# Kernel optimization log

Measured on AMD Instinct MI355X. Metric: run time of the kernel, lower is better.

The kernel has to match this reference:

```python
import jax, jax.numpy as jnp
import numpy as np
import math

B, T, H, W, D = 64, 512, 128, 128, 32


def _lin(k, out, inn):
    k1, k2 = jax.random.split(k)
    lim = 1.0 / np.sqrt(inn)
    return (jax.random.uniform(k1, (out, inn), jnp.float32, -lim, lim),
            jax.random.uniform(k2, (out,), jnp.float32, -lim, lim))


def setup_inputs() -> dict:
    key = jax.random.key(0)
    ks = jax.random.split(key, 12)
    ts = jnp.broadcast_to(jnp.linspace(0.0, 4.0 * math.pi, T, dtype=jnp.float32), (B, T))
    coef = lambda k: jax.random.normal(k, (B, T - 1, D), jnp.float32) * 0.1
    i_W0, i_b0 = _lin(ks[4], W, D)
    i_W1, i_b1 = _lin(ks[5], W, W)
    i_W2, i_b2 = _lin(ks[6], H, W)
    f_W0, f_b0 = _lin(ks[7], W, H)
    f_W1, f_b1 = _lin(ks[8], W, W)
    f_W2, f_b2 = _lin(ks[9], H * D, W)
    l_W, l_b = _lin(ks[10], 1, H)
    return dict(ts=ts,
                coeff_d=coef(ks[0]), coeff_c=coef(ks[1]), coeff_b=coef(ks[2]), coeff_a=coef(ks[3]),
                i_W0=i_W0, i_b0=i_b0, i_W1=i_W1, i_b1=i_b1, i_W2=i_W2, i_b2=i_b2,
                f_W0=f_W0, f_b0=f_b0, f_W1=f_W1, f_b1=f_b1, f_W2=f_W2, f_b2=f_b2,
                l_W=l_W, l_b=l_b)


def reference(ts, coeff_d, coeff_c, coeff_b, coeff_a,
              i_W0, i_b0, i_W1, i_b1, i_W2, i_b2,
              f_W0, f_b0, f_W1, f_b1, f_W2, f_b2,
              l_W, l_b):
    def initial_mlp(x):  # eqx.nn.MLP default: relu hidden, identity final
        x = jax.nn.relu(i_W0 @ x + i_b0)
        x = jax.nn.relu(i_W1 @ x + i_b1)
        return i_W2 @ x + i_b2

    def func_mlp(y):  # softplus hidden, tanh final, reshape (H, D)
        h = jax.nn.softplus(f_W0 @ y + f_b0)
        h = jax.nn.softplus(f_W1 @ h + f_b1)
        return jnp.tanh(f_W2 @ h + f_b2).reshape(H, D)

    def single(ts_i, d, c, b, a):
        dt = ts_i[1] - ts_i[0]
        y0 = initial_mlp(a[0])  # control.evaluate(ts[0]) = a[0] (frac=0 in first interval)

        def deriv(t):  # diffrax CubicInterpolation.derivative
            idx = jnp.clip(jnp.searchsorted(ts_i, t, side='right') - 1, 0, ts_i.shape[0] - 2)
            frac = t - ts_i[idx]
            return b[idx] + frac * (2.0 * c[idx] + frac * 3.0 * d[idx])

        def f(t, y):  # ControlTerm.to_ode() vf_prod with control=dt
            return (func_mlp(y) @ deriv(t)) * dt

        def step(carry, _):  # ralston_step_fn
            t0, y = carry
            k1 = f(t0, y)
            k2 = f(t0 + 0.5 * dt, y + 0.5 * k1)
            k3 = f(t0 + 0.75 * dt, y + 0.75 * k2)
            y1 = (2.0 / 9.0 * k1 + 1.0 / 3.0 * k2 + 4.0 / 9.0 * k3) * dt + y
            return (t0 + dt, y1), y1

        _, ys = jax.lax.scan(step, (ts_i[0], y0), None, length=ts_i.shape[0])
        return jax.nn.sigmoid(ys @ l_W[0] + l_b[0])  # (T,), evolving_out=True

    return jax.vmap(single)(ts, coeff_d, coeff_c, coeff_b, coeff_a)
```

## Files before the change

### kernel.cpp

```cpp
#include <hip/hip_runtime.h>
#include <hip/hip_bf16.h>

#define TT 512
#define BB 64
#define HH 128
#define WW 128
#define DD 32
#define NTHR 512
#define CSTRIDE 16352

#define SMEM_BYTES 86016

typedef __attribute__((ext_vector_type(8))) short short8;
typedef __attribute__((ext_vector_type(4))) float f32x4;

__device__ __forceinline__ float softplus_f(float x) {
    return fmaxf(x, 0.f) + __logf(1.f + __expf(-fabsf(x)));
}
__device__ __forceinline__ float fast_tanh(float x) {
    float ax = fabsf(x);
    float e  = __expf(-2.f * ax);
    float r  = (1.f - e) * __builtin_amdgcn_rcpf(1.f + e);
    return copysignf(r, x);
}
__device__ __forceinline__ short bf16rne(float x) {
    unsigned u = __float_as_uint(x);
    u += 0x7fffu + ((u >> 16) & 1u);
    return (short)(u >> 16);
}
__device__ __forceinline__ void store_l2(unsigned long long* p, unsigned long long v) {
    asm volatile("global_store_dwordx2 %0, %1, off sc0"
                 :: "v"(p), "v"(v) : "memory");
}
__device__ __forceinline__ unsigned long long load_l2(const unsigned long long* p) {
    unsigned long long v;
    asm volatile("global_load_dwordx2 %0, %1, off sc0\n\t"
                 "s_waitcnt vmcnt(0)"
                 : "=v"(v) : "v"(p) : "memory");
    return v;
}

__global__ __launch_bounds__(NTHR, 2)
void cde_kernel(const float* __restrict__ ts,
                const float* __restrict__ cd, const float* __restrict__ cc,
                const float* __restrict__ cb, const float* __restrict__ ca,
                const float* __restrict__ iW0, const float* __restrict__ ib0,
                const float* __restrict__ iW1, const float* __restrict__ ib1,
                const float* __restrict__ iW2, const float* __restrict__ ib2,
                const float* __restrict__ fW0, const float* __restrict__ fb0,
                const float* __restrict__ fW1, const float* __restrict__ fb1,
                const float* __restrict__ fW2, const float* __restrict__ fb2,
                const float* __restrict__ lW, const float* __restrict__ lb,
                unsigned* __restrict__ xcdctr,
                float* camb,
                unsigned long long* kslow,
                float* __restrict__ out)
{
    extern __shared__ float sm[];
    float* tss    = sm;
    float* ybuf   = tss + TT;
    float* dvec   = ybuf + 128;
    float* scr    = dvec + 96;
    float* klocal = scr + 256;
    short* ybf    = (short*)(klocal + 32);
    short* h1bf   = ybf + 128;
    short* h2bf   = h1bf + 128;
    int*   clm    = (int*)(h2bf + 128);

    const int tid  = threadIdx.x;
    const int lane = tid & 63;
    const int wv   = tid >> 6;
    const int quad = lane >> 4;
    const int qr   = lane & 15;

    if (tid == 0) {
        unsigned xcc;
        asm volatile("s_getreg_b32 %0, hwreg(HW_REG_XCC_ID)" : "=s"(xcc));
        xcc &= 7u;
        unsigned slot = atomicAdd(&xcdctr[xcc], 1u);
        clm[0] = (int)(xcc * 8u + (slot >> 2));
        clm[1] = (int)(slot & 3u);
    }
    __syncthreads();
    const int b = clm[0];
    const int m = clm[1];

    unsigned long long* kfast =
        (unsigned long long*)(camb + (size_t)b * CSTRIDE + 2048);

    const int cg = qr & 3;
    const int ct = (qr >> 2) & 1;
    const int rh = qr >> 3;
    const int dbase = ct * 16 + quad * 4 + rh * 2;

    for (int i = tid; i < TT; i += NTHR) tss[i] = ts[(size_t)b * TT + i];

    short8 afr[4][8];
    #pragma unroll
    for (int gi = 0; gi < 4; ++gi) {
        int g = m * 32 + wv * 4 + gi;
        #pragma unroll
        for (int t = 0; t < 2; ++t)
        #pragma unroll
        for (int K = 0; K < 4; ++K) {
            int row = g * 32 + t * 16 + qr;
            int col = K * 32 + quad * 8;
            const float* src = fW2 + (size_t)row * WW + col;
            short8 v;
            #pragma unroll
            for (int j = 0; j < 8; ++j) v[j] = bf16rne(src[j]);
            afr[gi][t * 4 + K] = v;
        }
    }
    short8 w0f[4], w1f[4];
    #pragma unroll
    for (int K = 0; K < 4; ++K) {
        int row = wv * 16 + qr;
        int col = K * 32 + quad * 8;
        const float* s0 = fW0 + (size_t)row * HH + col;
        const float* s1 = fW1 + (size_t)row * WW + col;
        short8 v0, v1;
        #pragma unroll
        for (int j = 0; j < 8; ++j) { v0[j] = bf16rne(s0[j]); v1[j] = bf16rne(s1[j]); }
        w0f[K] = v0; w1f[K] = v1;
    }
    const float fb0r = fb0[wv * 16 + quad * 4 + cg];
    const float fb1r = fb1[wv * 16 + quad * 4 + cg];
    const int   hrow = m * 32 + wv * 4 + cg;
    const float fb2a = fb2[hrow * 32 + dbase];
    const float fb2b = fb2[hrow * 32 + dbase + 1];

    __syncthreads();

    const float dt = tss[1] - tss[0];
    float t00 = tss[0];
    const size_t cstride = (size_t)CSTRIDE;
    const float* cdb = cd + (size_t)b * cstride;
    const float* ccb = cc + (size_t)b * cstride;
    const float* cbb = cb + (size_t)b * cstride;

    if (tid < HH) {
        const float* a0 = ca + (size_t)b * cstride;
        float acc = ib0[tid];
        #pragma unroll
        for (int k = 0; k < DD; ++k) acc += iW0[tid * DD + k] * a0[k];
        scr[tid] = fmaxf(acc, 0.f);
    }
    __syncthreads();
    if (tid < HH) {
        float acc = ib1[tid];
        for (int k = 0; k < WW; ++k) acc += iW1[tid * WW + k] * scr[k];
        scr[128 + tid] = fmaxf(acc, 0.f);
    }
    __syncthreads();
    float yreg = 0.f, k1r = 0.f, k2r = 0.f;
    if (tid < HH) {
        float acc = ib2[tid];
        for (int k = 0; k < WW; ++k) acc += iW2[tid * WW + k] * scr[128 + k];
        yreg = acc;
        ybuf[tid] = acc;
        ybf[tid]  = bf16rne(acc);
    }
    __syncthreads();

    float lwa = 0.f, lwb = 0.f, lbv = 0.f;
    if (wv == 0) { lwa = lW[lane]; lwb = lW[64 + lane]; lbv = lb[0]; }

    for (int s = 0; s < TT; ++s) {
        if (wv < 3) {
            float tv = t00 + ((wv == 0) ? 0.f : (wv == 1) ? 0.5f : 0.75f) * dt;
            int cnt = 0;
            #pragma unroll
            for (int ch = 0; ch < 8; ++ch)
                cnt += __popcll(__ballot(tss[ch * 64 + lane] <= tv));
            int idx = min(max(cnt - 1, 0), TT - 2);
            if (lane < DD) {
                float frac = tv - tss[idx];
                size_t o = (size_t)idx * DD + lane;
                dvec[wv * 32 + lane] =
                    cbb[o] + frac * (2.f * ccb[o] + frac * 3.f * cdb[o]);
            }
        }

        #pragma unroll 1
        for (int q = 0; q < 3; ++q) {
            const int gen = s * 3 + q + 1;
            const int buf = gen & 1;

            {
                f32x4 aA = {0.f, 0.f, 0.f, 0.f}, aB = {0.f, 0.f, 0.f, 0.f};
                short8 b0 = *(const short8*)(ybf + 0 * 32 + quad * 8);
                short8 b1 = *(const short8*)(ybf + 1 * 32 + quad * 8);
                short8 b2 = *(const short8*)(ybf + 2 * 32 + quad * 8);
                short8 b3 = *(const short8*)(ybf + 3 * 32 + quad * 8);
                aA = __builtin_amdgcn_mfma_f32_16x16x32_bf16(w0f[0], b0, aA, 0, 0, 0);
                aB = __builtin_amdgcn_mfma_f32_16x16x32_bf16(w0f[1], b1, aB, 0, 0, 0);
                aA = __builtin_amdgcn_mfma_f32_16x16x32_bf16(w0f[2], b2, aA, 0, 0, 0);
                aB = __builtin_amdgcn_mfma_f32_16x16x32_bf16(w0f[3], b3, aB, 0, 0, 0);
                f32x4 h = aA + aB;
                if (qr < 4) {
                    float v = (qr & 1) ? ((qr & 2) ? h[3] : h[1])
                                       : ((qr & 2) ? h[2] : h[0]);
                    h1bf[wv * 16 + quad * 4 + qr] = bf16rne(softplus_f(v + fb0r));
                }
            }
            __syncthreads();
            {
                f32x4 aA = {0.f, 0.f, 0.f, 0.f}, aB = {0.f, 0.f, 0.f, 0.f};
                short8 b0 = *(const short8*)(h1bf + 0 * 32 + quad * 8);
                short8 b1 = *(const short8*)(h1bf + 1 * 32 + quad * 8);
                short8 b2 = *(const short8*)(h1bf + 2 * 32 + quad * 8);
                short8 b3 = *(const short8*)(h1bf + 3 * 32 + quad * 8);
                aA = __builtin_amdgcn_mfma_f32_16x16x32_bf16(w1f[0], b0, aA, 0, 0, 0);
                aB = __builtin_amdgcn_mfma_f32_16x16x32_bf16(w1f[1], b1, aB, 0, 0, 0);
                aA = __builtin_amdgcn_mfma_f32_16x16x32_bf16(w1f[2], b2, aA, 0, 0, 0);
                aB = __builtin_amdgcn_mfma_f32_16x16x32_bf16(w1f[3], b3, aB, 0, 0, 0);
                f32x4 h = aA + aB;
                if (qr < 4) {
                    float v = (qr & 1) ? ((qr & 2) ? h[3] : h[1])
                                       : ((qr & 2) ? h[2] : h[0]);
                    h2bf[wv * 16 + quad * 4 + qr] = bf16rne(softplus_f(v + fb1r));
                }
            }
            __syncthreads();

            {
                short8 bfr[4];
                #pragma unroll
                for (int K = 0; K < 4; ++K)
                    bfr[K] = *(const short8*)(h2bf + K * 32 + quad * 8);
                f32x4 A0[4], A1[4];
                #pragma unroll
                for (int gi = 0; gi < 4; ++gi) {
                    f32x4 a0 = {0.f, 0.f, 0.f, 0.f};
                    f32x4 a1 = {0.f, 0.f, 0.f, 0.f};
                    a0 = __builtin_amdgcn_mfma_f32_16x16x32_bf16(afr[gi][0], bfr[0], a0, 0, 0, 0);
                    a0 = __builtin_amdgcn_mfma_f32_16x16x32_bf16(afr[gi][1], bfr[1], a0, 0, 0, 0);
                    a0 = __builtin_amdgcn_mfma_f32_16x16x32_bf16(afr[gi][2], bfr[2], a0, 0, 0, 0);
                    a0 = __builtin_amdgcn_mfma_f32_16x16x32_bf16(afr[gi][3], bfr[3], a0, 0, 0, 0);
                    a1 = __builtin_amdgcn_mfma_f32_16x16x32_bf16(afr[gi][4], bfr[0], a1, 0, 0, 0);
                    a1 = __builtin_amdgcn_mfma_f32_16x16x32_bf16(afr[gi][5], bfr[1], a1, 0, 0, 0);
                    a1 = __builtin_amdgcn_mfma_f32_16x16x32_bf16(afr[gi][6], bfr[2], a1, 0, 0, 0);
                    a1 = __builtin_amdgcn_mfma_f32_16x16x32_bf16(afr[gi][7], bfr[3], a1, 0, 0, 0);
                    A0[gi] = a0; A1[gi] = a1;
                }
                f32x4 s0a = (cg & 1) ? A0[1] : A0[0];
                f32x4 s0b = (cg & 1) ? A0[3] : A0[2];
                f32x4 s0  = (cg & 2) ? s0b : s0a;
                f32x4 s1a = (cg & 1) ? A1[1] : A1[0];
                f32x4 s1b = (cg & 1) ? A1[3] : A1[2];
                f32x4 s1  = (cg & 2) ? s1b : s1a;
                f32x4 st  = ct ? s1 : s0;
                float va = rh ? st[2] : st[0];
                float vb = rh ? st[3] : st[1];
                float2 dv = *(const float2*)(dvec + q * 32 + dbase);
                float p = fast_tanh(va + fb2a) * dv.x + fast_tanh(vb + fb2b) * dv.y;
                p += __shfl_xor(p, 8);
                p += __shfl_xor(p, 4);
                p += __shfl_xor(p, 16);
                p += __shfl_xor(p, 32);
                if (lane < 4) {
                    const float kval = p * dt;
                    const size_t off = (size_t)buf * HH + m * 32 + wv * 4 + lane;
                    unsigned long long pk =
                        ((unsigned long long)__float_as_uint(kval) << 32) | (unsigned)gen;
                    klocal[wv * 4 + lane] = kval;
                    store_l2(kfast + off, pk);
                    __hip_atomic_store(&kslow[(size_t)(buf * BB + b) * HH + m * 32 + wv * 4 + lane],
                                       pk, __ATOMIC_RELAXED, __HIP_MEMORY_SCOPE_AGENT);
                }
            }
            __syncthreads();

            if (tid < HH) {
                float kv;
                const int rel = tid - m * 32;
                if (rel >= 0 && rel < 32) {
                    kv = klocal[rel];
                } else {
                    unsigned long long v;
                    int it = 0;
                    for (;;) {
                        if ((it & 1) == 0) {
                            v = load_l2(kfast + (size_t)buf * HH + tid);
                        } else {
                            v = __hip_atomic_load(&kslow[(size_t)(buf * BB + b) * HH + tid],
                                                  __ATOMIC_RELAXED, __HIP_MEMORY_SCOPE_AGENT);
                        }
                        if ((unsigned)v == (unsigned)gen) break;
                        if (++it > 128) __builtin_amdgcn_s_sleep(1);
                    }
                    kv = __uint_as_float((unsigned)(v >> 32));
                }
                float nxt;
                if (q == 0)      { k1r = kv; nxt = yreg + 0.5f  * kv; }
                else if (q == 1) { k2r = kv; nxt = yreg + 0.75f * kv; }
                else {
                    nxt = yreg + dt * ((2.f/9.f) * k1r + (1.f/3.f) * k2r + (4.f/9.f) * kv);
                    yreg = nxt;
                    ybuf[tid] = nxt;
                }
                ybf[tid] = bf16rne(nxt);
            }
            __syncthreads();
        }

        if (m == 0 && wv == 0) {
            float p = ybuf[lane] * lwa + ybuf[64 + lane] * lwb;
            p += __shfl_xor(p, 1);  p += __shfl_xor(p, 2);  p += __shfl_xor(p, 4);
            p += __shfl_xor(p, 8);  p += __shfl_xor(p, 16); p += __shfl_xor(p, 32);
            if (lane == 0) out[(size_t)b * TT + s] = 1.f / (1.f + __expf(-(p + lbv)));
        }
        t00 += dt;
    }
}

extern "C" void kernel_launch(void* const* d_in, const int* in_sizes, int n_in,
                              void* d_out, int out_size, void* d_ws, size_t ws_size,
                              hipStream_t stream) {
    const float* ts  = (const float*)d_in[0];
    const float* cdp = (const float*)d_in[1];
    const float* ccp = (const float*)d_in[2];
    const float* cbp = (const float*)d_in[3];
    const float* cap = (const float*)d_in[4];
    const float* iW0 = (const float*)d_in[5];
    const float* ib0 = (const float*)d_in[6];
    const float* iW1 = (const float*)d_in[7];
    const float* ib1 = (const float*)d_in[8];
    const float* iW2 = (const float*)d_in[9];
    const float* ib2 = (const float*)d_in[10];
    const float* fW0 = (const float*)d_in[11];
    const float* fb0 = (const float*)d_in[12];
    const float* fW1 = (const float*)d_in[13];
    const float* fb1 = (const float*)d_in[14];
    const float* fW2 = (const float*)d_in[15];
    const float* fb2 = (const float*)d_in[16];
    const float* lW  = (const float*)d_in[17];
    const float* lb  = (const float*)d_in[18];
    float* out = (float*)d_out;

    unsigned* xcdctr = (unsigned*)d_ws;
    unsigned long long* kslow = (unsigned long long*)((char*)d_ws + 256);
    hipMemsetAsync(d_ws, 0, 256 + (size_t)2 * BB * HH * sizeof(unsigned long long), stream);

    hipFuncSetAttribute((const void*)cde_kernel,
                        hipFuncAttributeMaxDynamicSharedMemorySize, SMEM_BYTES);
    hipLaunchKernelGGL(cde_kernel, dim3(256), dim3(NTHR), SMEM_BYTES, stream,
                       ts, cdp, ccp, cbp, cap, iW0, ib0, iW1, ib1, iW2, ib2,
                       fW0, fb0, fW1, fb1, fW2, fb2, lW, lb, xcdctr,
                       (float*)cap, kslow, out);
}
```

Measured before the change: 3.558 ms.

## Replicate y state per wave and poll k values directly, removing two block barriers

Each wave now keeps its own copy of the 128-element y vector in registers and in a private LDS slab. Every wave polls all k values from the global exchange buffer, including its own block's values, and updates its copy itself. This removes the two __syncthreads per RK stage that surrounded the single-warp gather and update. The cost is eight times more global polling traffic per block and redundant y updates in every wave. Correctness still depends on wave-local LDS ordering and on the gen-tagged buffer double-buffering being safe without a block barrier.

New measurement: 10.40 ms. 192% more time.

```diff
diff --git a/kernel.cpp b/kernel.cpp
--- a/kernel.cpp
+++ b/kernel.cpp
@@ -32,12 +32,34 @@
     asm volatile("global_store_dwordx2 %0, %1, off sc0"
                  :: "v"(p), "v"(v) : "memory");
 }
-__device__ __forceinline__ unsigned long long load_l2(const unsigned long long* p) {
-    unsigned long long v;
-    asm volatile("global_load_dwordx2 %0, %1, off sc0\n\t"
-                 "s_waitcnt vmcnt(0)"
-                 : "=v"(v) : "v"(p) : "memory");
-    return v;
+
+__device__ __forceinline__ void poll_pair(const unsigned long long* f0,
+                                          const unsigned long long* s0,
+                                          unsigned gen, float& kv0, float& kv1) {
+    unsigned long long v0 = 0, v1 = 0;
+    bool d0 = false, d1 = false;
+    int it = 0;
+    for (;;) {
+        unsigned long long a, b;
+        asm volatile("global_load_dwordx2 %0, %2, off sc0\n\t"
+                     "global_load_dwordx2 %1, %3, off sc0\n\t"
+                     "s_waitcnt vmcnt(0)"
+                     : "=&v"(a), "=&v"(b)
+                     : "v"(f0), "v"(f0 + 64) : "memory");
+        if ((unsigned)a == gen) { v0 = a; d0 = true; }
+        if ((unsigned)b == gen) { v1 = b; d1 = true; }
+        if (d0 && d1) break;
+        if (++it > 24) {
+            a = __hip_atomic_load(s0,      __ATOMIC_RELAXED, __HIP_MEMORY_SCOPE_AGENT);
+            b = __hip_atomic_load(s0 + 64, __ATOMIC_RELAXED, __HIP_MEMORY_SCOPE_AGENT);
+            if ((unsigned)a == gen) { v0 = a; d0 = true; }
+            if ((unsigned)b == gen) { v1 = b; d1 = true; }
+            if (d0 && d1) break;
+            __builtin_amdgcn_s_sleep(1);
+        }
+    }
+    kv0 = __uint_as_float((unsigned)(v0 >> 32));
+    kv1 = __uint_as_float((unsigned)(v1 >> 32));
 }
 
 __global__ __launch_bounds__(NTHR, 2)
@@ -58,20 +80,20 @@
 {
     extern __shared__ float sm[];
     float* tss    = sm;
-    float* ybuf   = tss + TT;
-    float* dvec   = ybuf + 128;
+    float* dvec   = tss + TT;
     float* scr    = dvec + 96;
-    float* klocal = scr + 256;
-    short* ybf    = (short*)(klocal + 32);
-    short* h1bf   = ybf + 128;
+    float* yini   = scr + 256;
+    short* h1bf   = (short*)(yini + 128);
     short* h2bf   = h1bf + 128;
-    int*   clm    = (int*)(h2bf + 128);
+    short* ybp    = h2bf + 128;
+    int*   clm    = (int*)(ybp + 8 * 128);
 
     const int tid  = threadIdx.x;
     const int lane = tid & 63;
     const int wv   = tid >> 6;
     const int quad = lane >> 4;
     const int qr   = lane & 15;
+    short* myslab  = ybp + wv * 128;
 
     if (tid == 0) {
         unsigned xcc;
@@ -153,15 +175,18 @@
         scr[128 + tid] = fmaxf(acc, 0.f);
     }
     __syncthreads();
-    float yreg = 0.f, k1r = 0.f, k2r = 0.f;
     if (tid < HH) {
         float acc = ib2[tid];
         for (int k = 0; k < WW; ++k) acc += iW2[tid * WW + k] * scr[128 + k];
-        yreg = acc;
-        ybuf[tid] = acc;
-        ybf[tid]  = bf16rne(acc);
-    }
-    __syncthreads();
+        yini[tid] = acc;
+    }
+    __syncthreads();
+
+    float y0 = yini[lane];
+    float y1 = yini[lane + 64];
+    myslab[lane]      = bf16rne(y0);
+    myslab[lane + 64] = bf16rne(y1);
+    float k1a = 0.f, k1b = 0.f, k2a = 0.f, k2b = 0.f;
 
     float lwa = 0.f, lwb = 0.f, lbv = 0.f;
     if (wv == 0) { lwa = lW[lane]; lwb = lW[64 + lane]; lbv = lb[0]; }
@@ -189,10 +214,10 @@
 
             {
                 f32x4 aA = {0.f, 0.f, 0.f, 0.f}, aB = {0.f, 0.f, 0.f, 0.f};
-                short8 b0 = *(const short8*)(ybf + 0 * 32 + quad * 8);
-                short8 b1 = *(const short8*)(ybf + 1 * 32 + quad * 8);
-                short8 b2 = *(const short8*)(ybf + 2 * 32 + quad * 8);
-                short8 b3 = *(const short8*)(ybf + 3 * 32 + quad * 8);
+                short8 b0 = *(const short8*)(myslab + 0 * 32 + quad * 8);
+                short8 b1 = *(const short8*)(myslab + 1 * 32 + quad * 8);
+                short8 b2 = *(const short8*)(myslab + 2 * 32 + quad * 8);
+                short8 b3 = *(const short8*)(myslab + 3 * 32 + quad * 8);
                 aA = __builtin_amdgcn_mfma_f32_16x16x32_bf16(w0f[0], b0, aA, 0, 0, 0);
                 aB = __builtin_amdgcn_mfma_f32_16x16x32_bf16(w0f[1], b1, aB, 0, 0, 0);
                 aA = __builtin_amdgcn_mfma_f32_16x16x32_bf16(w0f[2], b2, aA, 0, 0, 0);
@@ -264,49 +289,30 @@
                     const size_t off = (size_t)buf * HH + m * 32 + wv * 4 + lane;
                     unsigned long long pk =
                         ((unsigned long long)__float_as_uint(kval) << 32) | (unsigned)gen;
-                    klocal[wv * 4 + lane] = kval;
                     store_l2(kfast + off, pk);
                     __hip_atomic_store(&kslow[(size_t)(buf * BB + b) * HH + m * 32 + wv * 4 + lane],
                                        pk, __ATOMIC_RELAXED, __HIP_MEMORY_SCOPE_AGENT);
                 }
             }
-            __syncthreads();
-
-            if (tid < HH) {
-                float kv;
-                const int rel = tid - m * 32;
-                if (rel >= 0 && rel < 32) {
-                    kv = klocal[rel];
-                } else {
-                    unsigned long long v;
-                    int it = 0;
-                    for (;;) {
-                        if ((it & 1) == 0) {
-                            v = load_l2(kfast + (size_t)buf * HH + tid);
-                        } else {
-                            v = __hip_atomic_load(&kslow[(size_t)(buf * BB + b) * HH + tid],
-                                                  __ATOMIC_RELAXED, __HIP_MEMORY_SCOPE_AGENT);
-                        }
-                        if ((unsigned)v == (unsigned)gen) break;
-                        if (++it > 128) __builtin_amdgcn_s_sleep(1);
-                    }
-                    kv = __uint_as_float((unsigned)(v >> 32));
-                }
-                float nxt;
-                if (q == 0)      { k1r = kv; nxt = yreg + 0.5f  * kv; }
-                else if (q == 1) { k2r = kv; nxt = yreg + 0.75f * kv; }
-                else {
-                    nxt = yreg + dt * ((2.f/9.f) * k1r + (1.f/3.f) * k2r + (4.f/9.f) * kv);
-                    yreg = nxt;
-                    ybuf[tid] = nxt;
-                }
-                ybf[tid] = bf16rne(nxt);
-            }
-            __syncthreads();
+
+            float kv0, kv1;
+            poll_pair(kfast + (size_t)buf * HH + lane,
+                      kslow + (size_t)(buf * BB + b) * HH + lane,
+                      (unsigned)gen, kv0, kv1);
+            float na, nb;
+            if (q == 0)      { k1a = kv0; k1b = kv1; na = y0 + 0.5f  * kv0; nb = y1 + 0.5f  * kv1; }
+            else if (q == 1) { k2a = kv0; k2b = kv1; na = y0 + 0.75f * kv0; nb = y1 + 0.75f * kv1; }
+            else {
+                na = y0 + dt * ((2.f/9.f) * k1a + (1.f/3.f) * k2a + (4.f/9.f) * kv0);
+                nb = y1 + dt * ((2.f/9.f) * k1b + (1.f/3.f) * k2b + (4.f/9.f) * kv1);
+                y0 = na; y1 = nb;
+            }
+            myslab[lane]      = bf16rne(na);
+            myslab[lane + 64] = bf16rne(nb);
         }
 
         if (m == 0 && wv == 0) {
-            float p = ybuf[lane] * lwa + ybuf[64 + lane] * lwb;
+            float p = y0 * lwa + y1 * lwb;
             p += __shfl_xor(p, 1);  p += __shfl_xor(p, 2);  p += __shfl_xor(p, 4);
             p += __shfl_xor(p, 8);  p += __shfl_xor(p, 16); p += __shfl_xor(p, 32);
             if (lane == 0) out[(size_t)b * TT + s] = 1.f / (1.f + __expf(-(p + lbv)));
```
